# Optimization experiments

Hardware: AMD Instinct MI355X
Metric: run time of the kernel (lower is better)

Reference implementation:

```python
import jax, jax.numpy as jnp
import numpy as np

B, T, D = 8, 1024, 1024
H, HS = 16, 64  # num_heads, head_size; H*HS == D


def setup_inputs() -> dict:
    key = jax.random.key(0)
    ks = jax.random.split(key, 5)
    scale = 0.02
    x = jax.random.normal(ks[0], (B, T, D), dtype=jnp.float32)
    Wq = jax.random.normal(ks[1], (H, D, HS), dtype=jnp.float32) * scale
    Wk = jax.random.normal(ks[2], (H, D, HS), dtype=jnp.float32) * scale
    Wv = jax.random.normal(ks[3], (H, D, HS), dtype=jnp.float32) * scale
    Wo = jax.random.normal(ks[4], (D, D), dtype=jnp.float32) * scale
    bo = jnp.zeros((D,), dtype=jnp.float32)
    return {"x": x, "Wq": Wq, "Wk": Wk, "Wv": Wv, "Wo": Wo, "bo": bo}


def reference(x, Wq, Wk, Wv, Wo, bo):
    # Per-head linear projections (bias-free, as in Head): [B,H,T,HS]
    q = jnp.einsum('btd,hds->bhts', x, Wq)
    k = jnp.einsum('btd,hds->bhts', x, Wk)
    v = jnp.einsum('btd,hds->bhts', x, Wv)
    # Scaled scores with causal mask: [B,H,T,T]
    scores = jnp.einsum('bhts,bhus->bhtu', q, k) * (HS ** -0.5)
    causal = jnp.tril(jnp.ones((T, T), dtype=bool))
    scores = jnp.where(causal, scores, jnp.finfo(scores.dtype).min)
    att = jax.nn.softmax(scores, axis=-1)
    # Weighted sum over values, then concat heads: [B,T,H*HS]
    out = jnp.einsum('bhtu,bhus->bhts', att, v)
    out = out.transpose(0, 2, 1, 3).reshape(B, T, H * HS)
    # Output projection (nn.Linear: y = x @ W^T + b)
    return out @ Wo.T + bo
```

## Files before the change

### kernel.cpp

```cpp
#include <hip/hip_runtime.h>
#include <hip/hip_bf16.h>

#define BBATCH 8
#define TSEQ   1024
#define DMODEL 1024
#define NHEAD  16
#define HSZ    64

typedef unsigned short ushort_t;
typedef __attribute__((ext_vector_type(8))) short short8;
typedef __attribute__((ext_vector_type(4))) float float4v;

__device__ __forceinline__ ushort_t f2bf(float f) {
    __hip_bfloat16 h = __float2bfloat16(f);
    return *reinterpret_cast<ushort_t*>(&h);
}
__device__ __forceinline__ ushort_t f2bf_fast(float f) {
    return (ushort_t)((__float_as_uint(f) + 0x8000u) >> 16);
}
__device__ __forceinline__ unsigned int pack_bf2(float lo, float hi) {
    unsigned int a = __float_as_uint(lo) + 0x8000u;
    unsigned int b = __float_as_uint(hi) + 0x8000u;
    return __builtin_amdgcn_perm(b, a, 0x07060302u);
}

__device__ __forceinline__ short8 cvt8(const float* f) {
    union { ushort_t u[8]; short8 v; } r;
    #pragma unroll
    for (int e = 0; e < 8; ++e) r.u[e] = f2bf(f[e]);
    return r.v;
}

__device__ __forceinline__ void async16(const ushort_t* g, ushort_t* l) {
    __builtin_amdgcn_global_load_lds(
        (const __attribute__((address_space(1))) unsigned int*)g,
        (__attribute__((address_space(3))) unsigned int*)l, 16, 0, 0);
}

__global__ __launch_bounds__(256) void cvt_f32_bf16(
    const float* __restrict__ src, ushort_t* __restrict__ dst)
{
    const size_t idx = ((size_t)blockIdx.x * 256 + threadIdx.x) * 16;
    float f[16];
    *(float4*)(f + 0)  = *(const float4*)(src + idx);
    *(float4*)(f + 4)  = *(const float4*)(src + idx + 4);
    *(float4*)(f + 8)  = *(const float4*)(src + idx + 8);
    *(float4*)(f + 12) = *(const float4*)(src + idx + 12);
    uint4 o0 = make_uint4(pack_bf2(f[0], f[1]),   pack_bf2(f[2], f[3]),
                          pack_bf2(f[4], f[5]),   pack_bf2(f[6], f[7]));
    uint4 o1 = make_uint4(pack_bf2(f[8], f[9]),   pack_bf2(f[10], f[11]),
                          pack_bf2(f[12], f[13]), pack_bf2(f[14], f[15]));
    *(uint4*)(dst + idx) = o0;
    *(uint4*)(dst + idx + 8) = o1;
}

__global__ __launch_bounds__(256) void pack_w(
    const float* __restrict__ Wq, const float* __restrict__ Wk,
    const float* __restrict__ Wv, ushort_t* __restrict__ WpT)
{
    __shared__ ushort_t L[64 * 72];
    const int tid = threadIdx.x;
    const int d0 = blockIdx.x * 64;
    const int wh = blockIdx.y;
    const int w = wh >> 4, h = wh & 15;
    const float* W = (w == 0 ? Wq : (w == 1 ? Wk : Wv)) + (size_t)h * DMODEL * HSZ;

    int dr = tid >> 2, sc = (tid & 3) * 16;
    const float4* src = (const float4*)(W + (size_t)(d0 + dr) * HSZ + sc);
    float f[16];
    *(float4*)(f + 0) = src[0]; *(float4*)(f + 4) = src[1];
    *(float4*)(f + 8) = src[2]; *(float4*)(f + 12) = src[3];
    *(short8*)(L + dr * 72 + sc)     = cvt8(f);
    *(short8*)(L + dr * 72 + sc + 8) = cvt8(f + 8);
    __syncthreads();

    int s = tid >> 2, dc = (tid & 3) * 16;
    union { ushort_t u[16]; short8 v[2]; } o;
    #pragma unroll
    for (int j = 0; j < 16; ++j) o.u[j] = L[(dc + j) * 72 + s];
    ushort_t* dst = WpT + (size_t)(w * 1024 + h * 64 + s) * DMODEL + d0 + dc;
    *(short8*)dst = o.v[0];
    *(short8*)(dst + 8) = o.v[1];
}

__global__ __launch_bounds__(256) void qkv_gemm(
    const ushort_t* __restrict__ Xb, const ushort_t* __restrict__ WpT,
    ushort_t* __restrict__ Qb, ushort_t* __restrict__ Kb, ushort_t* __restrict__ Vt)
{
    __shared__ ushort_t As[128 * 64];
    __shared__ ushort_t Bs[128 * 64];
    const int tid = threadIdx.x;
    const int wave = tid >> 6, lane = tid & 63;
    const int q = lane >> 4, cc = lane & 15;
    const int bid = blockIdx.x;
    const int xcd = bid & 7, local = bid >> 3;
    const int n_blk = local >> 3;
    const int m_blk = xcd * 8 + (local & 7);
    const int n0 = n_blk * 128, m0 = m_blk * 128;
    const int wm = wave >> 1, wn = wave & 1;
    const bool isV = (n0 >= 2048);

    const ushort_t* ag[4]; const ushort_t* bg[4]; int lo_[4];
    #pragma unroll
    for (int i = 0; i < 4; ++i) {
        int row = wave * 32 + i * 8 + (lane >> 3);
        int ch = (lane & 7) ^ (row & 7);
        ag[i] = Xb + (size_t)(m0 + row) * DMODEL + ch * 8;
        bg[i] = WpT + (size_t)(n0 + row) * DMODEL + ch * 8;
        lo_[i] = (wave * 32 + i * 8) * 64;
    }
    int aoff[4][2], boff[4][2];
    #pragma unroll
    for (int mt = 0; mt < 4; ++mt) {
        int row = wm * 64 + mt * 16 + cc;
        #pragma unroll
        for (int kt = 0; kt < 2; ++kt)
            aoff[mt][kt] = row * 64 + (((kt * 4 + q) ^ (row & 7)) * 8);
    }
    #pragma unroll
    for (int nt = 0; nt < 4; ++nt) {
        int row = wn * 64 + nt * 16 + cc;
        #pragma unroll
        for (int kt = 0; kt < 2; ++kt)
            boff[nt][kt] = row * 64 + (((kt * 4 + q) ^ (row & 7)) * 8);
    }

    float4v acc[4][4];
    #pragma unroll
    for (int a = 0; a < 4; ++a)
        #pragma unroll
        for (int b = 0; b < 4; ++b) acc[a][b] = (float4v){0.f, 0.f, 0.f, 0.f};

    for (int j = 0; j < 16; ++j) {
        #pragma unroll
        for (int i = 0; i < 4; ++i) {
            async16(ag[i], As + lo_[i]);
            async16(bg[i], Bs + lo_[i]);
            ag[i] += 64; bg[i] += 64;
        }
        __syncthreads();

        short8 av[4][2], bv[4][2];
        #pragma unroll
        for (int mt = 0; mt < 4; ++mt) {
            av[mt][0] = *(const short8*)(As + aoff[mt][0]);
            av[mt][1] = *(const short8*)(As + aoff[mt][1]);
        }
        #pragma unroll
        for (int nt = 0; nt < 4; ++nt) {
            bv[nt][0] = *(const short8*)(Bs + boff[nt][0]);
            bv[nt][1] = *(const short8*)(Bs + boff[nt][1]);
        }
        if (isV) {
            #pragma unroll
            for (int kt = 0; kt < 2; ++kt)
                #pragma unroll
                for (int mt = 0; mt < 4; ++mt)
                    #pragma unroll
                    for (int nt = 0; nt < 4; ++nt)
                        acc[mt][nt] = __builtin_amdgcn_mfma_f32_16x16x32_bf16(
                            av[mt][kt], bv[nt][kt], acc[mt][nt], 0, 0, 0);
        } else {
            #pragma unroll
            for (int kt = 0; kt < 2; ++kt)
                #pragma unroll
                for (int nt = 0; nt < 4; ++nt)
                    #pragma unroll
                    for (int mt = 0; mt < 4; ++mt)
                        acc[nt][mt] = __builtin_amdgcn_mfma_f32_16x16x32_bf16(
                            bv[nt][kt], av[mt][kt], acc[nt][mt], 0, 0, 0);
        }
        __syncthreads();
    }

    if (isV) {
        #pragma unroll
        for (int mt = 0; mt < 4; ++mt) {
            int m = m0 + wm * 64 + mt * 16 + q * 4;
            int b = m >> 10, t0_ = m & 1023;
            #pragma unroll
            for (int nt = 0; nt < 4; ++nt) {
                int n = n0 + wn * 64 + nt * 16 + cc;
                int h = (n >> 6) & 15, s = n & 63;
                size_t addr = (((size_t)(b * NHEAD + h)) * HSZ + s) * TSEQ + t0_;
                uint2 pk = make_uint2(pack_bf2(acc[mt][nt][0], acc[mt][nt][1]),
                                      pack_bf2(acc[mt][nt][2], acc[mt][nt][3]));
                *(uint2*)(Vt + addr) = pk;
            }
        }
    } else {
        const int nbase = n0 + wn * 64;
        ushort_t* Out = (nbase < 1024) ? Qb : Kb;
        const float osc = (nbase < 1024) ? 0.18033688011112042f : 1.0f;
        #pragma unroll
        for (int mt = 0; mt < 4; ++mt) {
            int m = m0 + wm * 64 + mt * 16 + cc;
            int b = m >> 10, t_ = m & 1023;
            #pragma unroll
            for (int nt = 0; nt < 4; ++nt) {
                int n = nbase + nt * 16 + q * 4;
                int h = (n >> 6) & 15, s0 = n & 63;
                size_t addr = (((size_t)(b * NHEAD + h)) * TSEQ + t_) * HSZ + s0;
                uint2 pk = make_uint2(
                    pack_bf2(acc[nt][mt][0] * osc, acc[nt][mt][1] * osc),
                    pack_bf2(acc[nt][mt][2] * osc, acc[nt][mt][3] * osc));
                *(uint2*)(Out + addr) = pk;
            }
        }
    }
}

__global__ __launch_bounds__(256) void attn(
    const ushort_t* __restrict__ Qb, const ushort_t* __restrict__ Kb,
    const ushort_t* __restrict__ Vt, ushort_t* __restrict__ Ob)
{
    __shared__ ushort_t Ks[2][64 * 64];
    __shared__ ushort_t VTs[2][64 * 64];
    __shared__ ushort_t Ps[4][32 * 72];
    const int tid = threadIdx.x;
    const int wave = tid >> 6, lane = tid & 63;
    const int q = lane >> 4, cc = lane & 15;
    const int bid = blockIdx.x;
    const int qt = 7 - (bid >> 7);
    const int bh = bid & 127;
    const size_t base = (size_t)bh * TSEQ * HSZ;
    const int J = 2 * qt + 2;

    const ushort_t* kg[2]; const ushort_t* vg[2]; int dmo[2];
    #pragma unroll
    for (int i = 0; i < 2; ++i) {
        int rr = wave * 16 + i * 8 + (lane >> 3);
        int ch = (lane & 7) ^ (rr & 7);
        kg[i] = Kb + base + (size_t)rr * HSZ + ch * 8;
        vg[i] = Vt + base + (size_t)rr * TSEQ + ch * 8;
        dmo[i] = (wave * 16 + i * 8) * 64;
    }

    short8 qf[2][2];
    #pragma unroll
    for (int tt = 0; tt < 2; ++tt) {
        const ushort_t* qp = Qb + base +
            (size_t)(qt * 128 + wave * 32 + tt * 16 + cc) * HSZ + q * 8;
        qf[tt][0] = *(const short8*)qp;
        qf[tt][1] = *(const short8*)(qp + 32);
    }

    int koff[4][2], poff[2][2];
    #pragma unroll
    for (int ut = 0; ut < 4; ++ut)
        #pragma unroll
        for (int kt = 0; kt < 2; ++kt)
            koff[ut][kt] = (ut * 16 + cc) * 64 + (((kt * 4 + q) ^ (cc & 7)) * 8);
    #pragma unroll
    for (int tt = 0; tt < 2; ++tt)
        #pragma unroll
        for (int kt = 0; kt < 2; ++kt)
            poff[tt][kt] = (tt * 16 + cc) * 72 + kt * 32 + q * 8;

    float4v oacc[2][4];
    #pragma unroll
    for (int tt = 0; tt < 2; ++tt)
        #pragma unroll
        for (int st = 0; st < 4; ++st) oacc[tt][st] = (float4v){0.f, 0.f, 0.f, 0.f};
    float lsum[2] = {0.f, 0.f};

    #pragma unroll
    for (int i = 0; i < 2; ++i) {
        async16(kg[i], &Ks[0][dmo[i]]);
        async16(vg[i], &VTs[0][dmo[i]]);
    }
    __syncthreads();

    for (int jt = 0; jt < J; ++jt) {
        const ushort_t* Kc = Ks[jt & 1];
        const ushort_t* Vc = VTs[jt & 1];
        if (jt + 1 < J) {
            int nb = (jt + 1) & 1;
            #pragma unroll
            for (int i = 0; i < 2; ++i) {
                async16(kg[i] + (size_t)(jt + 1) * 64 * HSZ, &Ks[nb][dmo[i]]);
                async16(vg[i] + (jt + 1) * 64, &VTs[nb][dmo[i]]);
            }
        }

        float4v sc[4][2];
        #pragma unroll
        for (int ut = 0; ut < 4; ++ut)
            #pragma unroll
            for (int tt = 0; tt < 2; ++tt) sc[ut][tt] = (float4v){0.f, 0.f, 0.f, 0.f};
        #pragma unroll
        for (int kt = 0; kt < 2; ++kt) {
            short8 kf[4];
            #pragma unroll
            for (int ut = 0; ut < 4; ++ut) kf[ut] = *(const short8*)(Kc + koff[ut][kt]);
            #pragma unroll
            for (int ut = 0; ut < 4; ++ut) {
                sc[ut][0] = __builtin_amdgcn_mfma_f32_16x16x32_bf16(
                    kf[ut], qf[0][kt], sc[ut][0], 0, 0, 0);
                sc[ut][1] = __builtin_amdgcn_mfma_f32_16x16x32_bf16(
                    kf[ut], qf[1][kt], sc[ut][1], 0, 0, 0);
            }
        }

        if ((jt >> 1) == qt) {
            #pragma unroll
            for (int tt = 0; tt < 2; ++tt) {
                const int tg = qt * 128 + wave * 32 + tt * 16 + cc;
                #pragma unroll
                for (int ut = 0; ut < 4; ++ut) {
                    float pv[4]; float ps = 0.f;
                    #pragma unroll
                    for (int rr = 0; rr < 4; ++rr) {
                        float p = exp2f(sc[ut][tt][rr]);
                        if ((jt * 64 + ut * 16 + q * 4 + rr) > tg) p = 0.f;
                        pv[rr] = p; ps += p;
                    }
                    lsum[tt] += ps;
                    *(uint2*)&Ps[wave][(tt * 16 + cc) * 72 + ut * 16 + q * 4] =
                        make_uint2(pack_bf2(pv[0], pv[1]), pack_bf2(pv[2], pv[3]));
                }
            }
        } else {
            #pragma unroll
            for (int tt = 0; tt < 2; ++tt) {
                #pragma unroll
                for (int ut = 0; ut < 4; ++ut) {
                    float pv[4]; float ps = 0.f;
                    #pragma unroll
                    for (int rr = 0; rr < 4; ++rr) {
                        float p = exp2f(sc[ut][tt][rr]);
                        pv[rr] = p; ps += p;
                    }
                    lsum[tt] += ps;
                    *(uint2*)&Ps[wave][(tt * 16 + cc) * 72 + ut * 16 + q * 4] =
                        make_uint2(pack_bf2(pv[0], pv[1]), pack_bf2(pv[2], pv[3]));
                }
            }
        }

        #pragma unroll
        for (int kt = 0; kt < 2; ++kt) {
            short8 pa0 = *(const short8*)&Ps[wave][poff[0][kt]];
            short8 pa1 = *(const short8*)&Ps[wave][poff[1][kt]];
            #pragma unroll
            for (int st = 0; st < 4; ++st) {
                short8 vf = *(const short8*)(Vc + koff[st][kt]);
                oacc[0][st] = __builtin_amdgcn_mfma_f32_16x16x32_bf16(
                    pa0, vf, oacc[0][st], 0, 0, 0);
                oacc[1][st] = __builtin_amdgcn_mfma_f32_16x16x32_bf16(
                    pa1, vf, oacc[1][st], 0, 0, 0);
            }
        }
        __syncthreads();
    }

    float inv[2];
    #pragma unroll
    for (int tt = 0; tt < 2; ++tt) {
        float l = lsum[tt];
        l += __shfl_xor(l, 16);
        l += __shfl_xor(l, 32);
        inv[tt] = 1.f / l;
    }
    const int b = bh >> 4, h = bh & 15;
    #pragma unroll
    for (int tt = 0; tt < 2; ++tt)
        #pragma unroll
        for (int rr = 0; rr < 4; ++rr) {
            float iv = __shfl(inv[tt], q * 4 + rr);
            int t = qt * 128 + wave * 32 + tt * 16 + q * 4 + rr;
            size_t rb = ((size_t)b * TSEQ + t) * DMODEL + h * HSZ;
            #pragma unroll
            for (int st = 0; st < 4; ++st)
                Ob[rb + st * 16 + cc] = f2bf_fast(oacc[tt][st][rr] * iv);
        }
}

__global__ __launch_bounds__(256) void oproj_gemm(
    const ushort_t* __restrict__ Obuf, const ushort_t* __restrict__ Wob,
    const float* __restrict__ bo, float* __restrict__ out)
{
    __shared__ ushort_t As[128 * 64];
    __shared__ ushort_t Bs[128 * 64];
    const int tid = threadIdx.x;
    const int wave = tid >> 6, lane = tid & 63;
    const int q = lane >> 4, cc = lane & 15;
    const int bid = blockIdx.x;
    const int xcd = bid & 7, local = bid >> 3;
    const int n0 = (local >> 3) * 128;
    const int m0 = (xcd * 8 + (local & 7)) * 128;
    const int wm = wave >> 1, wn = wave & 1;

    const ushort_t* ag[4]; const ushort_t* bg[4]; int lo_[4];
    #pragma unroll
    for (int i = 0; i < 4; ++i) {
        int row = wave * 32 + i * 8 + (lane >> 3);
        int ch = (lane & 7) ^ (row & 7);
        ag[i] = Obuf + (size_t)(m0 + row) * DMODEL + ch * 8;
        bg[i] = Wob + (size_t)(n0 + row) * DMODEL + ch * 8;
        lo_[i] = (wave * 32 + i * 8) * 64;
    }
    int aoff[4][2], boff[4][2];
    #pragma unroll
    for (int mt = 0; mt < 4; ++mt) {
        int row = wm * 64 + mt * 16 + cc;
        #pragma unroll
        for (int kt = 0; kt < 2; ++kt)
            aoff[mt][kt] = row * 64 + (((kt * 4 + q) ^ (row & 7)) * 8);
    }
    #pragma unroll
    for (int nt = 0; nt < 4; ++nt) {
        int row = wn * 64 + nt * 16 + cc;
        #pragma unroll
        for (int kt = 0; kt < 2; ++kt)
            boff[nt][kt] = row * 64 + (((kt * 4 + q) ^ (row & 7)) * 8);
    }

    float4v acc[4][4];
    #pragma unroll
    for (int a = 0; a < 4; ++a)
        #pragma unroll
        for (int b = 0; b < 4; ++b) acc[a][b] = (float4v){0.f, 0.f, 0.f, 0.f};

    for (int j = 0; j < 16; ++j) {
        #pragma unroll
        for (int i = 0; i < 4; ++i) {
            async16(ag[i], As + lo_[i]);
            async16(bg[i], Bs + lo_[i]);
            ag[i] += 64; bg[i] += 64;
        }
        __syncthreads();

        short8 av[4][2], bv[4][2];
        #pragma unroll
        for (int mt = 0; mt < 4; ++mt) {
            av[mt][0] = *(const short8*)(As + aoff[mt][0]);
            av[mt][1] = *(const short8*)(As + aoff[mt][1]);
        }
        #pragma unroll
        for (int nt = 0; nt < 4; ++nt) {
            bv[nt][0] = *(const short8*)(Bs + boff[nt][0]);
            bv[nt][1] = *(const short8*)(Bs + boff[nt][1]);
        }
        #pragma unroll
        for (int kt = 0; kt < 2; ++kt)
            #pragma unroll
            for (int mt = 0; mt < 4; ++mt)
                #pragma unroll
                for (int nt = 0; nt < 4; ++nt)
                    acc[mt][nt] = __builtin_amdgcn_mfma_f32_16x16x32_bf16(
                        av[mt][kt], bv[nt][kt], acc[mt][nt], 0, 0, 0);
        __syncthreads();
    }

    #pragma unroll
    for (int nt = 0; nt < 4; ++nt) {
        int n = n0 + wn * 64 + nt * 16 + cc;
        float bias = bo[n];
        #pragma unroll
        for (int mt = 0; mt < 4; ++mt)
            #pragma unroll
            for (int rr = 0; rr < 4; ++rr) {
                int m = m0 + wm * 64 + mt * 16 + q * 4 + rr;
                out[(size_t)m * DMODEL + n] = acc[mt][nt][rr] + bias;
            }
    }
}

extern "C" void kernel_launch(void* const* d_in, const int* in_sizes, int n_in,
                              void* d_out, int out_size, void* d_ws, size_t ws_size,
                              hipStream_t stream)
{
    const float* x  = (const float*)d_in[0];
    const float* Wq = (const float*)d_in[1];
    const float* Wk = (const float*)d_in[2];
    const float* Wv = (const float*)d_in[3];
    const float* Wo = (const float*)d_in[4];
    const float* bo = (const float*)d_in[5];
    float* out = (float*)d_out;

    const size_t SEG = (size_t)8 * 1024 * 1024;
    ushort_t* Qb  = (ushort_t*)d_ws;
    ushort_t* Kb  = Qb + SEG;
    ushort_t* Vtb = Kb + SEG;
    ushort_t* WpT = Vtb + SEG;
    ushort_t* Ob  = WpT;
    ushort_t* Xb  = (ushort_t*)d_out;
    ushort_t* Wob = Qb;

    cvt_f32_bf16<<<dim3(2048),    256, 0, stream>>>(x, Xb);
    pack_w      <<<dim3(16, 48),  256, 0, stream>>>(Wq, Wk, Wv, WpT);
    qkv_gemm    <<<dim3(1536),    256, 0, stream>>>(Xb, WpT, Qb, Kb, Vtb);
    attn        <<<dim3(1024),    256, 0, stream>>>(Qb, Kb, Vtb, Ob);
    cvt_f32_bf16<<<dim3(256),     256, 0, stream>>>(Wo, Wob);
    oproj_gemm  <<<dim3(512),     256, 0, stream>>>(Ob, Wob, bo, out);
}
```

Before: 231.6 us.

## Rewrite QKV GEMM with 256x256 tiles, double-buffered LDS and interleaved MFMA

The QKV projection GEMM moves from 128x128 tiles with 4 waves and a single LDS buffer to 256x256 tiles with 8 waves and two LDS buffers. Global-to-LDS async loads for the next k-tile are issued between MFMA phases, with explicit vmcnt waits, raw s_barriers and s_setprio. This is meant to hide load latency and raise data reuse per block. The costs are a 128 KB LDS footprint and a 128-float accumulator per thread. With only 384 blocks there are fewer blocks to spread across CUs, and register or occupancy pressure could hurt.

After: 253.9 us. 1.1x slower.

```diff
diff --git a/kernel.cpp b/kernel.cpp
--- a/kernel.cpp
+++ b/kernel.cpp
@@ -83,128 +83,203 @@
     *(short8*)(dst + 8) = o.v[1];
 }
 
-__global__ __launch_bounds__(256) void qkv_gemm(
+template<bool STG, int VW>
+__device__ __forceinline__ void ktile_step(
+    ushort_t* As, ushort_t* Bs,
+    const ushort_t* (&gA)[4], const ushort_t* (&gB)[4],
+    const int wave,
+    const int aoff0, const int aoff1, const int boff0, const int boff1,
+    float4v (&acc)[8][4])
+{
+    short8 avA[4][2], avB[4][2], bv[2][2];
+
+    #pragma unroll
+    for (int a = 0; a < 4; ++a) {
+        avA[a][0] = *(const short8*)(As + aoff0 + a * 1024);
+        avA[a][1] = *(const short8*)(As + aoff1 + a * 1024);
+    }
+    #pragma unroll
+    for (int b = 0; b < 2; ++b) {
+        bv[b][0] = *(const short8*)(Bs + boff0 + b * 1024);
+        bv[b][1] = *(const short8*)(Bs + boff1 + b * 1024);
+    }
+    __builtin_amdgcn_s_barrier();
+    __builtin_amdgcn_s_setprio(1);
+    #pragma unroll
+    for (int kth = 0; kth < 2; ++kth)
+        #pragma unroll
+        for (int a = 0; a < 4; ++a)
+            #pragma unroll
+            for (int b = 0; b < 2; ++b)
+                acc[a][b] = __builtin_amdgcn_mfma_f32_16x16x32_bf16(
+                    avA[a][kth], bv[b][kth], acc[a][b], 0, 0, 0);
+    __builtin_amdgcn_s_setprio(0);
+    __builtin_amdgcn_s_barrier();
+
+    #pragma unroll
+    for (int a = 0; a < 4; ++a) {
+        avB[a][0] = *(const short8*)(As + aoff0 + (a + 4) * 1024);
+        avB[a][1] = *(const short8*)(As + aoff1 + (a + 4) * 1024);
+    }
+    __builtin_amdgcn_s_barrier();
+    __builtin_amdgcn_s_setprio(1);
+    #pragma unroll
+    for (int kth = 0; kth < 2; ++kth)
+        #pragma unroll
+        for (int a = 0; a < 4; ++a)
+            #pragma unroll
+            for (int b = 0; b < 2; ++b)
+                acc[a + 4][b] = __builtin_amdgcn_mfma_f32_16x16x32_bf16(
+                    avB[a][kth], bv[b][kth], acc[a + 4][b], 0, 0, 0);
+    __builtin_amdgcn_s_setprio(0);
+    __builtin_amdgcn_s_barrier();
+
+    #pragma unroll
+    for (int b = 0; b < 2; ++b) {
+        bv[b][0] = *(const short8*)(Bs + boff0 + (b + 2) * 1024);
+        bv[b][1] = *(const short8*)(Bs + boff1 + (b + 2) * 1024);
+    }
+    __builtin_amdgcn_s_barrier();
+    __builtin_amdgcn_s_setprio(1);
+    #pragma unroll
+    for (int kth = 0; kth < 2; ++kth)
+        #pragma unroll
+        for (int a = 0; a < 4; ++a)
+            #pragma unroll
+            for (int b = 0; b < 2; ++b)
+                acc[a][b + 2] = __builtin_amdgcn_mfma_f32_16x16x32_bf16(
+                    avA[a][kth], bv[b][kth], acc[a][b + 2], 0, 0, 0);
+    __builtin_amdgcn_s_setprio(0);
+    __builtin_amdgcn_s_barrier();
+
+    if (STG) {
+        #pragma unroll
+        for (int i = 0; i < 4; ++i) {
+            async16(gA[i], As + i * 4096 + wave * 512);
+            async16(gB[i], Bs + i * 4096 + wave * 512);
+            gA[i] += 64; gB[i] += 64;
+        }
+    }
+    __builtin_amdgcn_s_barrier();
+    __builtin_amdgcn_s_setprio(1);
+    #pragma unroll
+    for (int kth = 0; kth < 2; ++kth)
+        #pragma unroll
+        for (int a = 0; a < 4; ++a)
+            #pragma unroll
+            for (int b = 0; b < 2; ++b)
+                acc[a + 4][b + 2] = __builtin_amdgcn_mfma_f32_16x16x32_bf16(
+                    avB[a][kth], bv[b][kth], acc[a + 4][b + 2], 0, 0, 0);
+    __builtin_amdgcn_s_setprio(0);
+    if (VW == 8)      asm volatile("s_waitcnt vmcnt(8)" ::: "memory");
+    else if (VW == 0) asm volatile("s_waitcnt vmcnt(0)" ::: "memory");
+    __builtin_amdgcn_s_barrier();
+}
+
+__global__ __launch_bounds__(512, 2) void qkv_gemm(
     const ushort_t* __restrict__ Xb, const ushort_t* __restrict__ WpT,
     ushort_t* __restrict__ Qb, ushort_t* __restrict__ Kb, ushort_t* __restrict__ Vt)
 {
-    __shared__ ushort_t As[128 * 64];
-    __shared__ ushort_t Bs[128 * 64];
+    __shared__ ushort_t As0[256 * 64];
+    __shared__ ushort_t Bs0[256 * 64];
+    __shared__ ushort_t As1[256 * 64];
+    __shared__ ushort_t Bs1[256 * 64];
+
     const int tid = threadIdx.x;
     const int wave = tid >> 6, lane = tid & 63;
     const int q = lane >> 4, cc = lane & 15;
+    const int wm = wave >> 2, wn = wave & 3;
+
     const int bid = blockIdx.x;
-    const int xcd = bid & 7, local = bid >> 3;
-    const int n_blk = local >> 3;
-    const int m_blk = xcd * 8 + (local & 7);
-    const int n0 = n_blk * 128, m0 = m_blk * 128;
-    const int wm = wave >> 1, wn = wave & 1;
-    const bool isV = (n0 >= 2048);
-
-    const ushort_t* ag[4]; const ushort_t* bg[4]; int lo_[4];
+    const int xcd = bid & 7, lo = bid >> 3;
+    const bool isV = (lo >= 32);
+    int tn, tm;
+    if (!isV) { tn = lo >> 2;        tm = xcd * 4 + (lo & 3); }
+    else      { int v = lo - 32; tn = v >> 2; tm = xcd * 4 + (v & 3); }
+    const int n0 = (isV ? 2048 : 0) + tn * 256;
+    const int m0 = tm * 256;
+
+    const ushort_t* pA = isV ? Xb + (size_t)m0 * DMODEL : WpT + (size_t)n0 * DMODEL;
+    const ushort_t* pB = isV ? WpT + (size_t)n0 * DMODEL : Xb + (size_t)m0 * DMODEL;
+
+    const int srow = lane >> 3;
+    const int chx = (lane & 7) ^ srow;
+    const ushort_t* gA[4]; const ushort_t* gB[4];
     #pragma unroll
     for (int i = 0; i < 4; ++i) {
-        int row = wave * 32 + i * 8 + (lane >> 3);
-        int ch = (lane & 7) ^ (row & 7);
-        ag[i] = Xb + (size_t)(m0 + row) * DMODEL + ch * 8;
-        bg[i] = WpT + (size_t)(n0 + row) * DMODEL + ch * 8;
-        lo_[i] = (wave * 32 + i * 8) * 64;
-    }
-    int aoff[4][2], boff[4][2];
-    #pragma unroll
-    for (int mt = 0; mt < 4; ++mt) {
-        int row = wm * 64 + mt * 16 + cc;
-        #pragma unroll
-        for (int kt = 0; kt < 2; ++kt)
-            aoff[mt][kt] = row * 64 + (((kt * 4 + q) ^ (row & 7)) * 8);
-    }
-    #pragma unroll
-    for (int nt = 0; nt < 4; ++nt) {
-        int row = wn * 64 + nt * 16 + cc;
-        #pragma unroll
-        for (int kt = 0; kt < 2; ++kt)
-            boff[nt][kt] = row * 64 + (((kt * 4 + q) ^ (row & 7)) * 8);
-    }
-
-    float4v acc[4][4];
-    #pragma unroll
-    for (int a = 0; a < 4; ++a)
+        int row = i * 64 + wave * 8 + srow;
+        gA[i] = pA + (size_t)row * DMODEL + chx * 8;
+        gB[i] = pB + (size_t)row * DMODEL + chx * 8;
+    }
+
+    const int c7 = cc & 7;
+    const int arow = wm * 128 + cc;
+    const int brow = wn * 64 + cc;
+    const int aoff0 = arow * 64 + ((q ^ c7) * 8);
+    const int aoff1 = arow * 64 + (((4 + q) ^ c7) * 8);
+    const int boff0 = brow * 64 + ((q ^ c7) * 8);
+    const int boff1 = brow * 64 + (((4 + q) ^ c7) * 8);
+
+    float4v acc[8][4];
+    #pragma unroll
+    for (int a = 0; a < 8; ++a)
         #pragma unroll
         for (int b = 0; b < 4; ++b) acc[a][b] = (float4v){0.f, 0.f, 0.f, 0.f};
 
-    for (int j = 0; j < 16; ++j) {
-        #pragma unroll
-        for (int i = 0; i < 4; ++i) {
-            async16(ag[i], As + lo_[i]);
-            async16(bg[i], Bs + lo_[i]);
-            ag[i] += 64; bg[i] += 64;
-        }
-        __syncthreads();
-
-        short8 av[4][2], bv[4][2];
-        #pragma unroll
-        for (int mt = 0; mt < 4; ++mt) {
-            av[mt][0] = *(const short8*)(As + aoff[mt][0]);
-            av[mt][1] = *(const short8*)(As + aoff[mt][1]);
-        }
-        #pragma unroll
-        for (int nt = 0; nt < 4; ++nt) {
-            bv[nt][0] = *(const short8*)(Bs + boff[nt][0]);
-            bv[nt][1] = *(const short8*)(Bs + boff[nt][1]);
-        }
-        if (isV) {
-            #pragma unroll
-            for (int kt = 0; kt < 2; ++kt)
-                #pragma unroll
-                for (int mt = 0; mt < 4; ++mt)
-                    #pragma unroll
-                    for (int nt = 0; nt < 4; ++nt)
-                        acc[mt][nt] = __builtin_amdgcn_mfma_f32_16x16x32_bf16(
-                            av[mt][kt], bv[nt][kt], acc[mt][nt], 0, 0, 0);
-        } else {
-            #pragma unroll
-            for (int kt = 0; kt < 2; ++kt)
-                #pragma unroll
-                for (int nt = 0; nt < 4; ++nt)
-                    #pragma unroll
-                    for (int mt = 0; mt < 4; ++mt)
-                        acc[nt][mt] = __builtin_amdgcn_mfma_f32_16x16x32_bf16(
-                            bv[nt][kt], av[mt][kt], acc[nt][mt], 0, 0, 0);
-        }
-        __syncthreads();
-    }
-
-    if (isV) {
-        #pragma unroll
-        for (int mt = 0; mt < 4; ++mt) {
-            int m = m0 + wm * 64 + mt * 16 + q * 4;
-            int b = m >> 10, t0_ = m & 1023;
-            #pragma unroll
-            for (int nt = 0; nt < 4; ++nt) {
-                int n = n0 + wn * 64 + nt * 16 + cc;
-                int h = (n >> 6) & 15, s = n & 63;
-                size_t addr = (((size_t)(b * NHEAD + h)) * HSZ + s) * TSEQ + t0_;
-                uint2 pk = make_uint2(pack_bf2(acc[mt][nt][0], acc[mt][nt][1]),
-                                      pack_bf2(acc[mt][nt][2], acc[mt][nt][3]));
+    #pragma unroll
+    for (int i = 0; i < 4; ++i) {
+        async16(gA[i], As0 + i * 4096 + wave * 512);
+        async16(gB[i], Bs0 + i * 4096 + wave * 512);
+        gA[i] += 64; gB[i] += 64;
+    }
+    #pragma unroll
+    for (int i = 0; i < 4; ++i) {
+        async16(gA[i], As1 + i * 4096 + wave * 512);
+        async16(gB[i], Bs1 + i * 4096 + wave * 512);
+        gA[i] += 64; gB[i] += 64;
+    }
+    asm volatile("s_waitcnt vmcnt(8)" ::: "memory");
+    __builtin_amdgcn_s_barrier();
+
+    #pragma unroll 1
+    for (int it = 0; it < 7; ++it) {
+        ktile_step<true, 8>(As0, Bs0, gA, gB, wave, aoff0, aoff1, boff0, boff1, acc);
+        ktile_step<true, 8>(As1, Bs1, gA, gB, wave, aoff0, aoff1, boff0, boff1, acc);
+    }
+    ktile_step<false, 0>(As0, Bs0, gA, gB, wave, aoff0, aoff1, boff0, boff1, acc);
+    ktile_step<false, -1>(As1, Bs1, gA, gB, wave, aoff0, aoff1, boff0, boff1, acc);
+
+    if (!isV) {
+        ushort_t* Out = (n0 < 1024) ? Qb : Kb;
+        const float osc = (n0 < 1024) ? 0.18033688011112042f : 1.0f;
+        #pragma unroll
+        for (int a = 0; a < 8; ++a) {
+            int nr = n0 + wm * 128 + a * 16 + q * 4;
+            int h = (nr >> 6) & 15, s0 = nr & 63;
+            #pragma unroll
+            for (int b = 0; b < 4; ++b) {
+                int mc = m0 + wn * 64 + b * 16 + cc;
+                int bb = mc >> 10, t = mc & 1023;
+                size_t addr = (((size_t)(bb * NHEAD + h)) * TSEQ + t) * HSZ + s0;
+                uint2 pk = make_uint2(
+                    pack_bf2(acc[a][b][0] * osc, acc[a][b][1] * osc),
+                    pack_bf2(acc[a][b][2] * osc, acc[a][b][3] * osc));
+                *(uint2*)(Out + addr) = pk;
+            }
+        }
+    } else {
+        #pragma unroll
+        for (int a = 0; a < 8; ++a) {
+            int mr = m0 + wm * 128 + a * 16 + q * 4;
+            int bb = mr >> 10, t0 = mr & 1023;
+            #pragma unroll
+            for (int b = 0; b < 4; ++b) {
+                int nc = n0 + wn * 64 + b * 16 + cc;
+                int h = (nc >> 6) & 15, s = nc & 63;
+                size_t addr = (((size_t)(bb * NHEAD + h)) * HSZ + s) * TSEQ + t0;
+                uint2 pk = make_uint2(pack_bf2(acc[a][b][0], acc[a][b][1]),
+                                      pack_bf2(acc[a][b][2], acc[a][b][3]));
                 *(uint2*)(Vt + addr) = pk;
-            }
-        }
-    } else {
-        const int nbase = n0 + wn * 64;
-        ushort_t* Out = (nbase < 1024) ? Qb : Kb;
-        const float osc = (nbase < 1024) ? 0.18033688011112042f : 1.0f;
-        #pragma unroll
-        for (int mt = 0; mt < 4; ++mt) {
-            int m = m0 + wm * 64 + mt * 16 + cc;
-            int b = m >> 10, t_ = m & 1023;
-            #pragma unroll
-            for (int nt = 0; nt < 4; ++nt) {
-                int n = nbase + nt * 16 + q * 4;
-                int h = (n >> 6) & 15, s0 = n & 63;
-                size_t addr = (((size_t)(b * NHEAD + h)) * TSEQ + t_) * HSZ + s0;
-                uint2 pk = make_uint2(
-                    pack_bf2(acc[nt][mt][0] * osc, acc[nt][mt][1] * osc),
-                    pack_bf2(acc[nt][mt][2] * osc, acc[nt][mt][3] * osc));
-                *(uint2*)(Out + addr) = pk;
             }
         }
     }
@@ -490,7 +565,7 @@
 
     cvt_f32_bf16<<<dim3(2048),    256, 0, stream>>>(x, Xb);
     pack_w      <<<dim3(16, 48),  256, 0, stream>>>(Wq, Wk, Wv, WpT);
-    qkv_gemm    <<<dim3(1536),    256, 0, stream>>>(Xb, WpT, Qb, Kb, Vtb);
+    qkv_gemm    <<<dim3(384),     512, 0, stream>>>(Xb, WpT, Qb, Kb, Vtb);
     attn        <<<dim3(1024),    256, 0, stream>>>(Qb, Kb, Vtb, Ob);
     cvt_f32_bf16<<<dim3(256),     256, 0, stream>>>(Wo, Wob);
     oproj_gemm  <<<dim3(512),     256, 0, stream>>>(Ob, Wob, bo, out);
```

## Restructure QKV GEMM with triple-buffered async LDS pipeline and larger tiles

Applied to the files above, without the earlier changes.

Rewrites the QKV projection GEMM to use 512-thread blocks with 128x256 tiles, K-step 32, and a three-stage LDS ring. Global-to-LDS async loads for the next stages are issued while MFMAs run on the current one, gated by explicit vmcnt waits and raw barriers instead of two syncthreads per step. It also sets wave priority around the MFMA bursts. The aim is to hide global load latency and cut barrier stalls, at the cost of more LDS per block and hand-managed waitcnt logic that is fragile.

New measurement: 231.2 us. No clear change (-0.2%).

```diff
diff --git a/kernel.cpp b/kernel.cpp
--- a/kernel.cpp
+++ b/kernel.cpp
@@ -35,6 +35,11 @@
     __builtin_amdgcn_global_load_lds(
         (const __attribute__((address_space(1))) unsigned int*)g,
         (__attribute__((address_space(3))) unsigned int*)l, 16, 0, 0);
+}
+
+template<int N> __device__ __forceinline__ void vwait() {
+    if constexpr (N == 3)      asm volatile("s_waitcnt vmcnt(3)" ::: "memory");
+    else if constexpr (N == 0) asm volatile("s_waitcnt vmcnt(0)" ::: "memory");
 }
 
 __global__ __launch_bounds__(256) void cvt_f32_bf16(
@@ -83,46 +88,78 @@
     *(short8*)(dst + 8) = o.v[1];
 }
 
-__global__ __launch_bounds__(256) void qkv_gemm(
+template<bool STG, int VW>
+__device__ __forceinline__ void kstep32(
+    const ushort_t* Ab, const ushort_t* Bb,
+    ushort_t* An, ushort_t* Bn,
+    const ushort_t*& gA, const ushort_t*& gB,
+    const int wave,
+    const int (&aoff)[4], const int (&boff)[4],
+    float4v (&acc)[4][4])
+{
+    short8 av[4], bv[4];
+    #pragma unroll
+    for (int a = 0; a < 4; ++a) av[a] = *(const short8*)(Ab + aoff[a]);
+    #pragma unroll
+    for (int b = 0; b < 4; ++b) bv[b] = *(const short8*)(Bb + boff[b]);
+    if (STG) {
+        async16(gA,                  An + wave * 512);
+        async16(gB,                  Bn + wave * 512);
+        async16(gB + 128 * DMODEL,   Bn + 4096 + wave * 512);
+        gA += 32; gB += 32;
+    }
+    __builtin_amdgcn_s_setprio(1);
+    #pragma unroll
+    for (int a = 0; a < 4; ++a)
+        #pragma unroll
+        for (int b = 0; b < 4; ++b)
+            acc[a][b] = __builtin_amdgcn_mfma_f32_16x16x32_bf16(
+                av[a], bv[b], acc[a][b], 0, 0, 0);
+    __builtin_amdgcn_s_setprio(0);
+    vwait<VW>();
+    __builtin_amdgcn_s_barrier();
+}
+
+__global__ __launch_bounds__(512, 2) void qkv_gemm(
     const ushort_t* __restrict__ Xb, const ushort_t* __restrict__ WpT,
     ushort_t* __restrict__ Qb, ushort_t* __restrict__ Kb, ushort_t* __restrict__ Vt)
 {
-    __shared__ ushort_t As[128 * 64];
-    __shared__ ushort_t Bs[128 * 64];
+    __shared__ ushort_t Ab[3][128 * 32];
+    __shared__ ushort_t Bb[3][256 * 32];
+
     const int tid = threadIdx.x;
     const int wave = tid >> 6, lane = tid & 63;
     const int q = lane >> 4, cc = lane & 15;
+    const int wm = wave >> 2, wn = wave & 3;
+
     const int bid = blockIdx.x;
-    const int xcd = bid & 7, local = bid >> 3;
-    const int n_blk = local >> 3;
-    const int m_blk = xcd * 8 + (local & 7);
-    const int n0 = n_blk * 128, m0 = m_blk * 128;
-    const int wm = wave >> 1, wn = wave & 1;
-    const bool isV = (n0 >= 2048);
-
-    const ushort_t* ag[4]; const ushort_t* bg[4]; int lo_[4];
-    #pragma unroll
-    for (int i = 0; i < 4; ++i) {
-        int row = wave * 32 + i * 8 + (lane >> 3);
-        int ch = (lane & 7) ^ (row & 7);
-        ag[i] = Xb + (size_t)(m0 + row) * DMODEL + ch * 8;
-        bg[i] = WpT + (size_t)(n0 + row) * DMODEL + ch * 8;
-        lo_[i] = (wave * 32 + i * 8) * 64;
-    }
-    int aoff[4][2], boff[4][2];
-    #pragma unroll
-    for (int mt = 0; mt < 4; ++mt) {
-        int row = wm * 64 + mt * 16 + cc;
-        #pragma unroll
-        for (int kt = 0; kt < 2; ++kt)
-            aoff[mt][kt] = row * 64 + (((kt * 4 + q) ^ (row & 7)) * 8);
-    }
-    #pragma unroll
-    for (int nt = 0; nt < 4; ++nt) {
-        int row = wn * 64 + nt * 16 + cc;
-        #pragma unroll
-        for (int kt = 0; kt < 2; ++kt)
-            boff[nt][kt] = row * 64 + (((kt * 4 + q) ^ (row & 7)) * 8);
+    const int xcd = bid & 7;
+    const bool isV = (bid >= 512);
+    int ta, tb;
+    if (!isV) {
+        int lo = bid >> 3;
+        ta = lo >> 2;
+        tb = xcd * 4 + (lo & 3);
+    } else {
+        int lo = (bid - 512) >> 3;
+        ta = xcd * 8 + (lo & 7);
+        tb = lo >> 3;
+    }
+    const ushort_t* pA = isV ? Xb  + (size_t)ta * 128 * DMODEL
+                             : WpT + (size_t)ta * 128 * DMODEL;
+    const ushort_t* pB = isV ? WpT + (size_t)(2048 + tb * 256) * DMODEL
+                             : Xb  + (size_t)tb * 256 * DMODEL;
+
+    const int srow = lane >> 2;
+    const int chx = (lane & 3) ^ (srow & 3);
+    const ushort_t* gA = pA + (size_t)(wave * 16 + srow) * DMODEL + chx * 8;
+    const ushort_t* gB = pB + (size_t)(wave * 16 + srow) * DMODEL + chx * 8;
+
+    int aoff[4], boff[4];
+    #pragma unroll
+    for (int f = 0; f < 4; ++f) {
+        aoff[f] = (wm * 64 + f * 16 + cc) * 32 + ((q ^ (cc & 3)) * 8);
+        boff[f] = (wn * 64 + f * 16 + cc) * 32 + ((q ^ (cc & 3)) * 8);
     }
 
     float4v acc[4][4];
@@ -131,80 +168,57 @@
         #pragma unroll
         for (int b = 0; b < 4; ++b) acc[a][b] = (float4v){0.f, 0.f, 0.f, 0.f};
 
-    for (int j = 0; j < 16; ++j) {
-        #pragma unroll
-        for (int i = 0; i < 4; ++i) {
-            async16(ag[i], As + lo_[i]);
-            async16(bg[i], Bs + lo_[i]);
-            ag[i] += 64; bg[i] += 64;
-        }
-        __syncthreads();
-
-        short8 av[4][2], bv[4][2];
-        #pragma unroll
-        for (int mt = 0; mt < 4; ++mt) {
-            av[mt][0] = *(const short8*)(As + aoff[mt][0]);
-            av[mt][1] = *(const short8*)(As + aoff[mt][1]);
-        }
-        #pragma unroll
-        for (int nt = 0; nt < 4; ++nt) {
-            bv[nt][0] = *(const short8*)(Bs + boff[nt][0]);
-            bv[nt][1] = *(const short8*)(Bs + boff[nt][1]);
-        }
-        if (isV) {
-            #pragma unroll
-            for (int kt = 0; kt < 2; ++kt)
-                #pragma unroll
-                for (int mt = 0; mt < 4; ++mt)
-                    #pragma unroll
-                    for (int nt = 0; nt < 4; ++nt)
-                        acc[mt][nt] = __builtin_amdgcn_mfma_f32_16x16x32_bf16(
-                            av[mt][kt], bv[nt][kt], acc[mt][nt], 0, 0, 0);
-        } else {
-            #pragma unroll
-            for (int kt = 0; kt < 2; ++kt)
-                #pragma unroll
-                for (int nt = 0; nt < 4; ++nt)
-                    #pragma unroll
-                    for (int mt = 0; mt < 4; ++mt)
-                        acc[nt][mt] = __builtin_amdgcn_mfma_f32_16x16x32_bf16(
-                            bv[nt][kt], av[mt][kt], acc[nt][mt], 0, 0, 0);
-        }
-        __syncthreads();
-    }
-
-    if (isV) {
-        #pragma unroll
-        for (int mt = 0; mt < 4; ++mt) {
-            int m = m0 + wm * 64 + mt * 16 + q * 4;
-            int b = m >> 10, t0_ = m & 1023;
-            #pragma unroll
-            for (int nt = 0; nt < 4; ++nt) {
-                int n = n0 + wn * 64 + nt * 16 + cc;
-                int h = (n >> 6) & 15, s = n & 63;
-                size_t addr = (((size_t)(b * NHEAD + h)) * HSZ + s) * TSEQ + t0_;
-                uint2 pk = make_uint2(pack_bf2(acc[mt][nt][0], acc[mt][nt][1]),
-                                      pack_bf2(acc[mt][nt][2], acc[mt][nt][3]));
+    async16(gA,                Ab[0] + wave * 512);
+    async16(gB,                Bb[0] + wave * 512);
+    async16(gB + 128 * DMODEL, Bb[0] + 4096 + wave * 512);
+    gA += 32; gB += 32;
+    async16(gA,                Ab[1] + wave * 512);
+    async16(gB,                Bb[1] + wave * 512);
+    async16(gB + 128 * DMODEL, Bb[1] + 4096 + wave * 512);
+    gA += 32; gB += 32;
+    vwait<3>();
+    __builtin_amdgcn_s_barrier();
+
+    #pragma unroll 1
+    for (int it = 0; it < 10; ++it) {
+        kstep32<true, 3>(Ab[0], Bb[0], Ab[2], Bb[2], gA, gB, wave, aoff, boff, acc);
+        kstep32<true, 3>(Ab[1], Bb[1], Ab[0], Bb[0], gA, gB, wave, aoff, boff, acc);
+        kstep32<true, 3>(Ab[2], Bb[2], Ab[1], Bb[1], gA, gB, wave, aoff, boff, acc);
+    }
+    kstep32<false, 0>(Ab[0], Bb[0], Ab[2], Bb[2], gA, gB, wave, aoff, boff, acc);
+    kstep32<false, -1>(Ab[1], Bb[1], Ab[0], Bb[0], gA, gB, wave, aoff, boff, acc);
+
+    if (!isV) {
+        ushort_t* Out = (ta < 8) ? Qb : Kb;
+        const float osc = (ta < 8) ? 0.18033688011112042f : 1.0f;
+        const int h = ((ta * 128 + wm * 64) >> 6) & 15;
+        #pragma unroll
+        for (int b = 0; b < 4; ++b) {
+            int mc = tb * 256 + wn * 64 + b * 16 + cc;
+            int bb = mc >> 10, t = mc & 1023;
+            size_t rb = (((size_t)(bb * NHEAD + h)) * TSEQ + t) * HSZ;
+            #pragma unroll
+            for (int a = 0; a < 4; ++a) {
+                int s0 = a * 16 + q * 4;
+                uint2 pk = make_uint2(
+                    pack_bf2(acc[a][b][0] * osc, acc[a][b][1] * osc),
+                    pack_bf2(acc[a][b][2] * osc, acc[a][b][3] * osc));
+                *(uint2*)(Out + rb + s0) = pk;
+            }
+        }
+    } else {
+        #pragma unroll
+        for (int b = 0; b < 4; ++b) {
+            int nc = tb * 256 + wn * 64 + b * 16 + cc;
+            int h = nc >> 6, s = nc & 63;
+            #pragma unroll
+            for (int a = 0; a < 4; ++a) {
+                int mr = ta * 128 + wm * 64 + a * 16 + q * 4;
+                int bb = mr >> 10, t0 = mr & 1023;
+                size_t addr = (((size_t)(bb * NHEAD + h)) * HSZ + s) * TSEQ + t0;
+                uint2 pk = make_uint2(pack_bf2(acc[a][b][0], acc[a][b][1]),
+                                      pack_bf2(acc[a][b][2], acc[a][b][3]));
                 *(uint2*)(Vt + addr) = pk;
-            }
-        }
-    } else {
-        const int nbase = n0 + wn * 64;
-        ushort_t* Out = (nbase < 1024) ? Qb : Kb;
-        const float osc = (nbase < 1024) ? 0.18033688011112042f : 1.0f;
-        #pragma unroll
-        for (int mt = 0; mt < 4; ++mt) {
-            int m = m0 + wm * 64 + mt * 16 + cc;
-            int b = m >> 10, t_ = m & 1023;
-            #pragma unroll
-            for (int nt = 0; nt < 4; ++nt) {
-                int n = nbase + nt * 16 + q * 4;
-                int h = (n >> 6) & 15, s0 = n & 63;
-                size_t addr = (((size_t)(b * NHEAD + h)) * TSEQ + t_) * HSZ + s0;
-                uint2 pk = make_uint2(
-                    pack_bf2(acc[nt][mt][0] * osc, acc[nt][mt][1] * osc),
-                    pack_bf2(acc[nt][mt][2] * osc, acc[nt][mt][3] * osc));
-                *(uint2*)(Out + addr) = pk;
             }
         }
     }
@@ -490,7 +504,7 @@
 
     cvt_f32_bf16<<<dim3(2048),    256, 0, stream>>>(x, Xb);
     pack_w      <<<dim3(16, 48),  256, 0, stream>>>(Wq, Wk, Wv, WpT);
-    qkv_gemm    <<<dim3(1536),    256, 0, stream>>>(Xb, WpT, Qb, Kb, Vtb);
+    qkv_gemm    <<<dim3(768),     512, 0, stream>>>(Xb, WpT, Qb, Kb, Vtb);
     attn        <<<dim3(1024),    256, 0, stream>>>(Qb, Kb, Vtb, Ob);
     cvt_f32_bf16<<<dim3(256),     256, 0, stream>>>(Wo, Wob);
     oproj_gemm  <<<dim3(512),     256, 0, stream>>>(Ob, Wob, bo, out);
```
